# Kernel tuning notes

Measured on AMD Instinct MI355X. Metric: run time of the kernel, lower is better.

Reference implementation:

```python
import jax, jax.numpy as jnp
import numpy as np

B, S, H = 2, 2048, 1024
NH, HD = 16, 64
WIN = 256
EPS = 1e-5


def _layernorm(x, g, b):
    # normalize over last dim (head_dim)
    m = jnp.mean(x, axis=-1, keepdims=True)
    v = jnp.mean((x - m) ** 2, axis=-1, keepdims=True)
    return (x - m) * jax.lax.rsqrt(v + EPS) * g + b


def setup_inputs() -> dict:
    key = jax.random.key(0)
    ks = jax.random.split(key, 6)
    scale = 1.0 / np.sqrt(2.0 * H)  # ~ xavier_uniform with gain 1/sqrt(2)
    inp = {
        "x": jax.random.normal(ks[0], (B, S, H), dtype=jnp.float32),
        "Wq": jax.random.normal(ks[1], (H, H), dtype=jnp.float32) * scale,
        "bq": jnp.zeros((H,), jnp.float32),
        "Wk": jax.random.normal(ks[2], (H, H), dtype=jnp.float32) * scale,
        "bk": jnp.zeros((H,), jnp.float32),
        "Wv": jax.random.normal(ks[3], (H, H), dtype=jnp.float32) * scale,
        "bv": jnp.zeros((H,), jnp.float32),
        "Wo": jax.random.normal(ks[4], (H, H), dtype=jnp.float32) * scale,
        "bo": jnp.zeros((H,), jnp.float32),
        "ln_q_w": jnp.ones((HD,), jnp.float32),
        "ln_q_b": jnp.zeros((HD,), jnp.float32),
        "ln_k_w": jnp.ones((HD,), jnp.float32),
        "ln_k_b": jnp.zeros((HD,), jnp.float32),
    }
    return inp


def reference(x, Wq, bq, Wk, bk, Wv, bv, Wo, bo, ln_q_w, ln_q_b, ln_k_w, ln_k_b):
    b, s, _ = x.shape
    # projections (torch Linear: x @ W.T + b)
    q = (x @ Wq.T + bq).reshape(b, s, NH, HD)
    k = (x @ Wk.T + bk).reshape(b, s, NH, HD)
    v = (x @ Wv.T + bv).reshape(b, s, NH, HD)
    # QK layernorm over head_dim
    q = _layernorm(q, ln_q_w, ln_q_b)
    k = _layernorm(k, ln_k_w, ln_k_b)
    # scores [b, h, s, s]
    scores = jnp.einsum("bqhd,bkhd->bhqk", q, k) / np.sqrt(HD).astype(np.float32)
    i = jnp.arange(s)[:, None]
    j = jnp.arange(s)[None, :]
    mask = (j <= i) & (i - j <= WIN)
    scores = jnp.where(mask[None, None], scores, -jnp.inf)
    probs = jax.nn.softmax(scores, axis=-1)
    out = jnp.einsum("bhqk,bkhd->bqhd", probs, v).reshape(b, s, NH * HD)
    return out @ Wo.T + bo
```

## Files before the change

### kernel.cpp

```cpp
#include <hip/hip_runtime.h>
#include <hip/hip_bf16.h>
#include <cstdint>

typedef __hip_bfloat16 bf16;
typedef __attribute__((ext_vector_type(8))) short s16x8;
typedef __attribute__((ext_vector_type(4))) float f32x4;

#define NB_B 2
#define NB_S 2048
#define NB_H 1024
#define NB_NH 16
#define NB_HD 64
#define NB_WIN 256
#define NTOK 4096

static __device__ __forceinline__ unsigned pack_bf16(float a, float b) {
    bf16 ta = __float2bfloat16(a), tb = __float2bfloat16(b);
    return (unsigned)*(unsigned short*)&ta | ((unsigned)*(unsigned short*)&tb << 16);
}
static __device__ __forceinline__ unsigned short bf16u(float a) {
    bf16 t = __float2bfloat16(a);
    return *(unsigned short*)&t;
}

#define VMCNT(n) asm volatile("s_waitcnt vmcnt(" #n ")" ::: "memory")
#define SBAR __builtin_amdgcn_s_barrier()
#define LGKM0 do { asm volatile("s_waitcnt lgkmcnt(0)" ::: "memory"); \
                   __builtin_amdgcn_sched_barrier(0); } while (0)

__global__ void k_castall(const float* __restrict__ x, const float* __restrict__ Wq,
                          const float* __restrict__ Wk, const float* __restrict__ Wv,
                          const float* __restrict__ Wo,
                          bf16* __restrict__ xb, bf16* __restrict__ wqkvb,
                          bf16* __restrict__ wob) {
    int idx = blockIdx.x * blockDim.x + threadIdx.x;
    const float* in; bf16* out; int i;
    if (idx < 1048576)        { in = x;  out = xb;              i = idx * 4; }
    else if (idx < 1310720)   { in = Wq; out = wqkvb;           i = (idx - 1048576) * 4; }
    else if (idx < 1572864)   { in = Wk; out = wqkvb + 1048576; i = (idx - 1310720) * 4; }
    else if (idx < 1835008)   { in = Wv; out = wqkvb + 2097152; i = (idx - 1572864) * 4; }
    else                      { in = Wo; out = wob;             i = (idx - 1835008) * 4; }
    const float4 v = *(const float4*)(in + i);
    ushort4 u;
    u.x = bf16u(v.x); u.y = bf16u(v.y); u.z = bf16u(v.z); u.w = bf16u(v.w);
    *(ushort4*)((unsigned short*)out + i) = u;
}

#define GQ_STAGE(AD, BD, KT)                                                         \
    do {                                                                             \
        _Pragma("unroll")                                                            \
        for (int it_ = 0; it_ < 2; ++it_) {                                          \
            int c_ = it_ * 256 + tid;                                                \
            int row_ = c_ >> 2, pc_ = c_ & 3;                                        \
            int col_ = pc_ << 3;                                                     \
            __builtin_amdgcn_global_load_lds(                                        \
                (const __attribute__((address_space(1))) void*)(Ap + (size_t)(m0 + row_) * 1024 + (KT) + col_), \
                (__attribute__((address_space(3))) void*)((AD) + c_ * 8), 16, 0, 0); \
            __builtin_amdgcn_global_load_lds(                                        \
                (const __attribute__((address_space(1))) void*)(Bp + (size_t)(n0 + row_) * 1024 + (KT) + col_), \
                (__attribute__((address_space(3))) void*)((BD) + c_ * 8), 16, 0, 0); \
        }                                                                            \
        __builtin_amdgcn_sched_barrier(0);                                           \
    } while (0)

#define GQ_COMPUTE(AS, BS)                                                           \
    do {                                                                             \
        s16x8 af_[4], bf_[4];                                                        \
        _Pragma("unroll")                                                            \
        for (int mi_ = 0; mi_ < 4; ++mi_)                                            \
            af_[mi_] = *(const s16x8*)&(AS)[(wr * 64 + mi_ * 16 + q) * 32 + g * 8];  \
        _Pragma("unroll")                                                            \
        for (int ni_ = 0; ni_ < 4; ++ni_)                                            \
            bf_[ni_] = *(const s16x8*)&(BS)[(wc * 64 + ni_ * 16 + q) * 32 + g * 8];  \
        LGKM0;                                                                       \
        __builtin_amdgcn_s_setprio(1);                                               \
        _Pragma("unroll")                                                            \
        for (int mi_ = 0; mi_ < 4; ++mi_)                                            \
            _Pragma("unroll")                                                        \
            for (int ni_ = 0; ni_ < 4; ++ni_)                                        \
                acc[mi_][ni_] = __builtin_amdgcn_mfma_f32_16x16x32_bf16(             \
                    af_[mi_], bf_[ni_], acc[mi_][ni_], 0, 0, 0);                     \
        __builtin_amdgcn_s_setprio(0);                                               \
    } while (0)

#define GQ_MAINLOOP                                                                  \
    GQ_STAGE(As0, Bs0, 0);                                                           \
    GQ_STAGE(As1, Bs1, 32);                                                          \
    for (int i_ = 0; i_ < 15; ++i_) {                                                \
        const int kt_ = i_ * 64;                                                     \
        VMCNT(4); SBAR;                                                              \
        GQ_COMPUTE(As0, Bs0);                                                        \
        SBAR;                                                                        \
        GQ_STAGE(As0, Bs0, kt_ + 64);                                                \
        VMCNT(4); SBAR;                                                              \
        GQ_COMPUTE(As1, Bs1);                                                        \
        SBAR;                                                                        \
        GQ_STAGE(As1, Bs1, kt_ + 96);                                                \
    }                                                                                \
    VMCNT(4); SBAR;                                                                  \
    GQ_COMPUTE(As0, Bs0);                                                            \
    VMCNT(0); SBAR;                                                                  \
    GQ_COMPUTE(As1, Bs1)

__global__ __launch_bounds__(256, 4) void k_gemm_qkv(const bf16* __restrict__ Ap,
                                                  const bf16* __restrict__ Bp,
                                                  const float* __restrict__ bq,
                                                  const float* __restrict__ bk,
                                                  const float* __restrict__ bv,
                                                  const float* __restrict__ lqw,
                                                  const float* __restrict__ lqb,
                                                  const float* __restrict__ lkw,
                                                  const float* __restrict__ lkb,
                                                  bf16* __restrict__ qbuf,
                                                  bf16* __restrict__ kbuf,
                                                  bf16* __restrict__ vtb) {
    __shared__ bf16 As0[128 * 32], As1[128 * 32];
    __shared__ bf16 Bs0[128 * 32], Bs1[128 * 32];
    const int tid = threadIdx.x;
    const int lane = tid & 63;
    const int w = tid >> 6;
    const int wr = w >> 1, wc = w & 1;

    const int orig = blockIdx.y * gridDim.x + blockIdx.x;
    const int wk = (orig & 7) * 96 + (orig >> 3);
    const int m0 = (wk / 24) * 128, n0 = (wk % 24) * 128;

    const int g = lane >> 4, q = lane & 15;

    f32x4 acc[4][4] = {};

    GQ_MAINLOOP;

    const int col0 = n0 + wc * 64;
    const int hh = col0 >> 6;
    const int csub = col0 & 1023;
    const float* bias = (hh < 16) ? bq : (hh < 32) ? bk : bv;

    float bcol[4];
#pragma unroll
    for (int ni = 0; ni < 4; ++ni) bcol[ni] = bias[csub + ni * 16 + q];
#pragma unroll
    for (int mi = 0; mi < 4; ++mi)
#pragma unroll
        for (int ni = 0; ni < 4; ++ni)
#pragma unroll
            for (int r = 0; r < 4; ++r) acc[mi][ni][r] += bcol[ni];

    if (hh < 32) {
        const float* gwa = (hh < 16) ? lqw : lkw;
        const float* gba = (hh < 16) ? lqb : lkb;
        float gam[4], bet[4];
#pragma unroll
        for (int ni = 0; ni < 4; ++ni) {
            gam[ni] = gwa[ni * 16 + q];
            bet[ni] = gba[ni * 16 + q];
        }
        bf16* outp = (hh < 16) ? qbuf : kbuf;
#pragma unroll
        for (int mi = 0; mi < 4; ++mi)
#pragma unroll
            for (int r = 0; r < 4; ++r) {
                float s1 = acc[mi][0][r] + acc[mi][1][r] + acc[mi][2][r] + acc[mi][3][r];
                float s2 = acc[mi][0][r] * acc[mi][0][r] + acc[mi][1][r] * acc[mi][1][r]
                         + acc[mi][2][r] * acc[mi][2][r] + acc[mi][3][r] * acc[mi][3][r];
#pragma unroll
                for (int mm = 1; mm < 16; mm <<= 1) {
                    s1 += __shfl_xor(s1, mm, 64);
                    s2 += __shfl_xor(s2, mm, 64);
                }
                float mean = s1 * (1.f / 64.f);
                float var = s2 * (1.f / 64.f) - mean * mean;
                float rs = rsqrtf(var + 1e-5f);
                int token = m0 + wr * 64 + mi * 16 + g * 4 + r;
#pragma unroll
                for (int ni = 0; ni < 4; ++ni) {
                    float y = (acc[mi][ni][r] - mean) * rs * gam[ni] + bet[ni];
                    outp[(size_t)token * 1024 + csub + ni * 16 + q] = __float2bfloat16(y);
                }
            }
    } else {
        const int b = m0 >> 11;
        const int bh = b * 16 + (csub >> 6);
        const int sbase0 = (m0 & 2047) + wr * 64 + g * 4;
#pragma unroll
        for (int mi = 0; mi < 4; ++mi) {
            const int sb = sbase0 + mi * 16;
#pragma unroll
            for (int ni = 0; ni < 4; ++ni) {
                const int d = ni * 16 + q;
                ushort4 u;
                u.x = bf16u(acc[mi][ni][0]); u.y = bf16u(acc[mi][ni][1]);
                u.z = bf16u(acc[mi][ni][2]); u.w = bf16u(acc[mi][ni][3]);
                *(ushort4*)(vtb + ((size_t)bh * 64 + d) * 2048 + sb) = u;
            }
        }
    }
}

#define GO_STAGE(AD, BD, KT)                                                         \
    do {                                                                             \
        _Pragma("unroll")                                                            \
        for (int it_ = 0; it_ < 2; ++it_) {                                          \
            int c_ = it_ * 256 + tid;                                                \
            int row_ = c_ >> 2, pc_ = c_ & 3;                                        \
            int col_ = pc_ << 3;                                                     \
            __builtin_amdgcn_global_load_lds(                                        \
                (const __attribute__((address_space(1))) void*)(Ap + (size_t)(m0 + row_) * 1024 + (KT) + col_), \
                (__attribute__((address_space(3))) void*)((AD) + c_ * 8), 16, 0, 0); \
        }                                                                            \
        {                                                                            \
            int row_ = tid >> 2, pc_ = tid & 3;                                      \
            int col_ = pc_ << 3;                                                     \
            __builtin_amdgcn_global_load_lds(                                        \
                (const __attribute__((address_space(1))) void*)(Bp + (size_t)(n0 + row_) * 1024 + (KT) + col_), \
                (__attribute__((address_space(3))) void*)((BD) + tid * 8), 16, 0, 0); \
        }                                                                            \
        __builtin_amdgcn_sched_barrier(0);                                           \
    } while (0)

#define GO_COMPUTE(AS, BS)                                                           \
    do {                                                                             \
        s16x8 af_[4], bf_[2];                                                        \
        _Pragma("unroll")                                                            \
        for (int mi_ = 0; mi_ < 4; ++mi_)                                            \
            af_[mi_] = *(const s16x8*)&(AS)[(wr * 64 + mi_ * 16 + q) * 32 + g * 8];  \
        _Pragma("unroll")                                                            \
        for (int ni_ = 0; ni_ < 2; ++ni_)                                            \
            bf_[ni_] = *(const s16x8*)&(BS)[(wc * 32 + ni_ * 16 + q) * 32 + g * 8];  \
        LGKM0;                                                                       \
        __builtin_amdgcn_s_setprio(1);                                               \
        _Pragma("unroll")                                                            \
        for (int mi_ = 0; mi_ < 4; ++mi_)                                            \
            _Pragma("unroll")                                                        \
            for (int ni_ = 0; ni_ < 2; ++ni_)                                        \
                acc[mi_][ni_] = __builtin_amdgcn_mfma_f32_16x16x32_bf16(             \
                    af_[mi_], bf_[ni_], acc[mi_][ni_], 0, 0, 0);                     \
        __builtin_amdgcn_s_setprio(0);                                               \
    } while (0)

#define GO_MAINLOOP                                                                  \
    GO_STAGE(As0, Bs0, 0);                                                           \
    GO_STAGE(As1, Bs1, 32);                                                          \
    for (int i_ = 0; i_ < 15; ++i_) {                                                \
        const int kt_ = i_ * 64;                                                     \
        VMCNT(3); SBAR;                                                              \
        GO_COMPUTE(As0, Bs0);                                                        \
        SBAR;                                                                        \
        GO_STAGE(As0, Bs0, kt_ + 64);                                                \
        VMCNT(3); SBAR;                                                              \
        GO_COMPUTE(As1, Bs1);                                                        \
        SBAR;                                                                        \
        GO_STAGE(As1, Bs1, kt_ + 96);                                                \
    }                                                                                \
    VMCNT(3); SBAR;                                                                  \
    GO_COMPUTE(As0, Bs0);                                                            \
    VMCNT(0); SBAR;                                                                  \
    GO_COMPUTE(As1, Bs1)

__global__ __launch_bounds__(256, 4) void k_gemm_out(const bf16* __restrict__ Ap,
                                                  const bf16* __restrict__ Bp,
                                                  const float* __restrict__ bias,
                                                  float* __restrict__ Cv) {
    __shared__ bf16 As0[128 * 32], As1[128 * 32];
    __shared__ bf16 Bs0[64 * 32], Bs1[64 * 32];
    const int tid = threadIdx.x;
    const int lane = tid & 63;
    const int w = tid >> 6;
    const int wr = w >> 1, wc = w & 1;

    const int orig = blockIdx.y * gridDim.x + blockIdx.x;
    const int wk = (orig & 7) * 64 + (orig >> 3);
    const int m0 = (wk / 16) * 128, n0 = (wk % 16) * 64;

    const int g = lane >> 4, q = lane & 15;

    f32x4 acc[4][2] = {};

    GO_MAINLOOP;

#pragma unroll
    for (int mi = 0; mi < 4; ++mi)
#pragma unroll
        for (int ni = 0; ni < 2; ++ni) {
            int colg = n0 + wc * 32 + ni * 16 + q;
            float bcol = bias[colg];
#pragma unroll
            for (int r = 0; r < 4; ++r) {
                int rowg = m0 + wr * 64 + mi * 16 + g * 4 + r;
                Cv[(size_t)rowg * 1024 + colg] = acc[mi][ni][r] + bcol;
            }
        }
}

#undef GQ_STAGE
#undef GQ_COMPUTE
#undef GQ_MAINLOOP
#undef GO_STAGE
#undef GO_COMPUTE
#undef GO_MAINLOOP

__global__ __launch_bounds__(256) void k_attn(const bf16* __restrict__ qb,
                                              const bf16* __restrict__ kb,
                                              const bf16* __restrict__ vt,
                                              bf16* __restrict__ att) {
    __shared__ bf16 Ks[2][32 * 64];
    __shared__ bf16 Vs[2][64 * 32];

    const int orig = blockIdx.y * gridDim.x + blockIdx.x;
    const int wk = (orig & 7) * 128 + (orig >> 3);
    const int q0 = (wk & 31) * 64;
    const int bh = wk >> 5;

    const int b = bh >> 4, h = bh & 15;
    const int tid = threadIdx.x;
    const int w = tid >> 6;
    const int lane = tid & 63;
    const int g = lane >> 4, qi = lane & 15;
    const int qw0 = q0 + w * 16;
    const int iq = qw0 + qi;

    const size_t qbase = ((size_t)(b * 2048 + iq)) * 1024 + h * 64 + g * 8;
    s16x8 bq0 = *(const s16x8*)(qb + qbase);
    s16x8 bq1 = *(const s16x8*)(qb + qbase + 32);

    f32x4 o[4] = {};
    float lp = 0.f;

    int jmin = q0 - NB_WIN; if (jmin < 0) jmin = 0;
    const int c0 = jmin >> 5;
    const int c1 = (q0 + 63) >> 5;

    const int krow = tid >> 3, kpc = tid & 7;
    const int kcol = ((kpc ^ (krow & 7)) << 3);
    const int vrow = tid >> 2, vpc = tid & 3;
    const int vcol = ((vpc ^ (vrow & 3)) << 3);
    const bf16* kbase = kb + ((size_t)(b * 2048 + krow)) * 1024 + h * 64 + kcol;
    const bf16* vbase = vt + ((size_t)bh * 64 + vrow) * 2048 + vcol;

    __builtin_amdgcn_global_load_lds(
        (const __attribute__((address_space(1))) void*)(kbase + (size_t)(c0 * 32) * 1024),
        (__attribute__((address_space(3))) void*)(&Ks[0][tid * 8]), 16, 0, 0);
    __builtin_amdgcn_global_load_lds(
        (const __attribute__((address_space(1))) void*)(vbase + c0 * 32),
        (__attribute__((address_space(3))) void*)(&Vs[0][tid * 8]), 16, 0, 0);

    int buf = 0;
    for (int c = c0; c <= c1; ++c) {
        const int ks = c * 32;
        if (c < c1) {
            const int ksn = ks + 32;
            __builtin_amdgcn_global_load_lds(
                (const __attribute__((address_space(1))) void*)(kbase + (size_t)ksn * 1024),
                (__attribute__((address_space(3))) void*)(&Ks[buf ^ 1][tid * 8]), 16, 0, 0);
            __builtin_amdgcn_global_load_lds(
                (const __attribute__((address_space(1))) void*)(vbase + ksn),
                (__attribute__((address_space(3))) void*)(&Vs[buf ^ 1][tid * 8]), 16, 0, 0);
            __builtin_amdgcn_sched_barrier(0);
            VMCNT(2);
        } else {
            VMCNT(0);
        }
        SBAR;

        if (ks + 31 >= qw0 - NB_WIN && ks <= qw0 + 15) {
            const int ch0 = ((g ^ (qi & 7)) << 3);
            const bf16* kr0 = &Ks[buf][qi * 64];
            const bf16* kr1 = &Ks[buf][(16 + qi) * 64];
            s16x8 a00 = *(const s16x8*)(kr0 + ch0);
            s16x8 a01 = *(const s16x8*)(kr0 + (ch0 ^ 32));
            s16x8 a10 = *(const s16x8*)(kr1 + ch0);
            s16x8 a11 = *(const s16x8*)(kr1 + (ch0 ^ 32));

            f32x4 s0 = {}, s1 = {};
            s0 = __builtin_amdgcn_mfma_f32_16x16x32_bf16(a00, bq0, s0, 0, 0, 0);
            s0 = __builtin_amdgcn_mfma_f32_16x16x32_bf16(a01, bq1, s0, 0, 0, 0);
            s1 = __builtin_amdgcn_mfma_f32_16x16x32_bf16(a10, bq0, s1, 0, 0, 0);
            s1 = __builtin_amdgcn_mfma_f32_16x16x32_bf16(a11, bq1, s1, 0, 0, 0);

            float p0[4], p1[4];
#pragma unroll
            for (int r = 0; r < 4; ++r) {
                int j0 = ks + 4 * g + r, j1 = j0 + 16;
                p0[r] = ((unsigned)(iq - j0) <= (unsigned)NB_WIN)
                            ? __expf(s0[r] * 0.125f - 8.f) : 0.f;
                p1[r] = ((unsigned)(iq - j1) <= (unsigned)NB_WIN)
                            ? __expf(s1[r] * 0.125f - 8.f) : 0.f;
                lp += p0[r] + p1[r];
            }
            unsigned P0 = pack_bf16(p0[0], p0[1]), P1 = pack_bf16(p0[2], p0[3]);
            unsigned Q0 = pack_bf16(p1[0], p1[1]), Q1 = pack_bf16(p1[2], p1[3]);

            const int srcA = qi + (g & 1) * 32;
            const int srcB = srcA + 16;
            unsigned tP0a = __shfl((int)P0, srcA, 64), tQ0a = __shfl((int)Q0, srcA, 64);
            unsigned tP1a = __shfl((int)P1, srcA, 64), tQ1a = __shfl((int)Q1, srcA, 64);
            unsigned tP0b = __shfl((int)P0, srcB, 64), tQ0b = __shfl((int)Q0, srcB, 64);
            unsigned tP1b = __shfl((int)P1, srcB, 64), tQ1b = __shfl((int)Q1, srcB, 64);
            union { s16x8 v; unsigned u[4]; } pa;
            pa.u[0] = (g < 2) ? tP0a : tQ0a;
            pa.u[1] = (g < 2) ? tP1a : tQ1a;
            pa.u[2] = (g < 2) ? tP0b : tQ0b;
            pa.u[3] = (g < 2) ? tP1b : tQ1b;

            const int chv = ((g ^ (qi & 3)) << 3);
#pragma unroll
            for (int db = 0; db < 4; ++db) {
                s16x8 bv = *(const s16x8*)&Vs[buf][(db * 16 + qi) * 32 + chv];
                o[db] = __builtin_amdgcn_mfma_f32_16x16x32_bf16(pa.v, bv, o[db], 0, 0, 0);
            }
        }

        SBAR;
        buf ^= 1;
    }

    float l2 = lp + __shfl_xor(lp, 16, 64);
    float lf = l2 + __shfl_xor(l2, 32, 64);
    float lr[4];
#pragma unroll
    for (int r = 0; r < 4; ++r) lr[r] = __shfl(lf, 4 * g + r, 64);

#pragma unroll
    for (int db = 0; db < 4; ++db)
#pragma unroll
        for (int r = 0; r < 4; ++r) {
            float vlu = o[db][r] / lr[r];
            att[((size_t)(b * 2048 + qw0 + 4 * g + r)) * 1024 + h * 64 + db * 16 + qi] =
                __float2bfloat16(vlu);
        }
}

extern "C" void kernel_launch(void* const* d_in, const int* in_sizes, int n_in,
                              void* d_out, int out_size, void* d_ws, size_t ws_size,
                              hipStream_t stream) {
    const float* x   = (const float*)d_in[0];
    const float* Wq  = (const float*)d_in[1];
    const float* bq  = (const float*)d_in[2];
    const float* Wk  = (const float*)d_in[3];
    const float* bk  = (const float*)d_in[4];
    const float* Wv  = (const float*)d_in[5];
    const float* bv  = (const float*)d_in[6];
    const float* Wo  = (const float*)d_in[7];
    const float* bo  = (const float*)d_in[8];
    const float* lqw = (const float*)d_in[9];
    const float* lqb = (const float*)d_in[10];
    const float* lkw = (const float*)d_in[11];
    const float* lkb = (const float*)d_in[12];

    char* ws = (char*)d_ws;
    bf16* xb    = (bf16*)(ws + 0);
    bf16* wqkvb = (bf16*)(ws + 8388608);
    bf16* wob   = (bf16*)(ws + 14680064);
    bf16* qbuf  = (bf16*)(ws + 16777216);
    bf16* kbuf  = (bf16*)(ws + 25165824);
    bf16* vtb   = (bf16*)(ws + 33554432);
    bf16* attb  = (bf16*)(ws + 41943040);

    k_castall<<<8192, 256, 0, stream>>>(x, Wq, Wk, Wv, Wo, xb, wqkvb, wob);

    k_gemm_qkv<<<dim3(24, 32), 256, 0, stream>>>(xb, wqkvb, bq, bk, bv,
                                                 lqw, lqb, lkw, lkb,
                                                 qbuf, kbuf, vtb);

    k_attn<<<dim3(32, 32), 256, 0, stream>>>(qbuf, kbuf, vtb, attb);

    k_gemm_out<<<dim3(16, 32), 256, 0, stream>>>(attb, wob, bo, (float*)d_out);
}
```

Before: 90.27 us.

## Triple-buffer GEMM LDS pipeline and XOR-swizzle tiles to avoid bank conflicts

Both the QKV and output-projection GEMMs move from a double-buffered to a triple-buffered LDS ring. The next tile load is issued before computing the current one, which keeps more global loads in flight. The global-to-LDS copy and the fragment reads now use an XOR swizzle on the 16-byte chunk index to cut LDS bank conflicts. The extra LDS per block lowers the QKV kernel's occupancy bound from 4 to 3 blocks, and the ring index arithmetic adds some loop overhead.

```diff
diff --git a/kernel.cpp b/kernel.cpp
--- a/kernel.cpp
+++ b/kernel.cpp
@@ -52,7 +52,7 @@
         for (int it_ = 0; it_ < 2; ++it_) {                                          \
             int c_ = it_ * 256 + tid;                                                \
             int row_ = c_ >> 2, pc_ = c_ & 3;                                        \
-            int col_ = pc_ << 3;                                                     \
+            int col_ = (pc_ ^ ((row_ >> 1) & 3)) << 3;                               \
             __builtin_amdgcn_global_load_lds(                                        \
                 (const __attribute__((address_space(1))) void*)(Ap + (size_t)(m0 + row_) * 1024 + (KT) + col_), \
                 (__attribute__((address_space(3))) void*)((AD) + c_ * 8), 16, 0, 0); \
@@ -65,13 +65,14 @@
 
 #define GQ_COMPUTE(AS, BS)                                                           \
     do {                                                                             \
+        const int chv_ = (g ^ ((q >> 1) & 3)) << 3;                                  \
         s16x8 af_[4], bf_[4];                                                        \
         _Pragma("unroll")                                                            \
         for (int mi_ = 0; mi_ < 4; ++mi_)                                            \
-            af_[mi_] = *(const s16x8*)&(AS)[(wr * 64 + mi_ * 16 + q) * 32 + g * 8];  \
+            af_[mi_] = *(const s16x8*)&(AS)[(wr * 64 + mi_ * 16 + q) * 32 + chv_];   \
         _Pragma("unroll")                                                            \
         for (int ni_ = 0; ni_ < 4; ++ni_)                                            \
-            bf_[ni_] = *(const s16x8*)&(BS)[(wc * 64 + ni_ * 16 + q) * 32 + g * 8];  \
+            bf_[ni_] = *(const s16x8*)&(BS)[(wc * 64 + ni_ * 16 + q) * 32 + chv_];   \
         LGKM0;                                                                       \
         __builtin_amdgcn_s_setprio(1);                                               \
         _Pragma("unroll")                                                            \
@@ -83,26 +84,28 @@
         __builtin_amdgcn_s_setprio(0);                                               \
     } while (0)
 
-#define GQ_MAINLOOP                                                                  \
-    GQ_STAGE(As0, Bs0, 0);                                                           \
-    GQ_STAGE(As1, Bs1, 32);                                                          \
-    for (int i_ = 0; i_ < 15; ++i_) {                                                \
-        const int kt_ = i_ * 64;                                                     \
+#define GQ_MAINLOOP(NT)                                                              \
+    GQ_STAGE(Asb + 0 * ABUF, Bsb + 0 * BBUF, 0);                                     \
+    GQ_STAGE(Asb + 1 * ABUF, Bsb + 1 * BBUF, 32);                                    \
+    {                                                                                \
+        int bc_ = 0, bs_ = 2;                                                        \
+        for (int t_ = 0; t_ < (NT) - 2; ++t_) {                                      \
+            GQ_STAGE(Asb + bs_ * ABUF, Bsb + bs_ * BBUF, (t_ + 2) * 32);             \
+            VMCNT(8); SBAR;                                                          \
+            GQ_COMPUTE(Asb + bc_ * ABUF, Bsb + bc_ * BBUF);                          \
+            SBAR;                                                                    \
+            bc_ = (bc_ + 1 == 3) ? 0 : bc_ + 1;                                      \
+            bs_ = (bs_ + 1 == 3) ? 0 : bs_ + 1;                                      \
+        }                                                                            \
         VMCNT(4); SBAR;                                                              \
-        GQ_COMPUTE(As0, Bs0);                                                        \
+        GQ_COMPUTE(Asb + bc_ * ABUF, Bsb + bc_ * BBUF);                              \
         SBAR;                                                                        \
-        GQ_STAGE(As0, Bs0, kt_ + 64);                                                \
-        VMCNT(4); SBAR;                                                              \
-        GQ_COMPUTE(As1, Bs1);                                                        \
-        SBAR;                                                                        \
-        GQ_STAGE(As1, Bs1, kt_ + 96);                                                \
-    }                                                                                \
-    VMCNT(4); SBAR;                                                                  \
-    GQ_COMPUTE(As0, Bs0);                                                            \
-    VMCNT(0); SBAR;                                                                  \
-    GQ_COMPUTE(As1, Bs1)
-
-__global__ __launch_bounds__(256, 4) void k_gemm_qkv(const bf16* __restrict__ Ap,
+        bc_ = (bc_ + 1 == 3) ? 0 : bc_ + 1;                                          \
+        VMCNT(0); SBAR;                                                              \
+        GQ_COMPUTE(Asb + bc_ * ABUF, Bsb + bc_ * BBUF);                              \
+    }
+
+__global__ __launch_bounds__(256, 3) void k_gemm_qkv(const bf16* __restrict__ Ap,
                                                   const bf16* __restrict__ Bp,
                                                   const float* __restrict__ bq,
                                                   const float* __restrict__ bk,
@@ -114,8 +117,9 @@
                                                   bf16* __restrict__ qbuf,
                                                   bf16* __restrict__ kbuf,
                                                   bf16* __restrict__ vtb) {
-    __shared__ bf16 As0[128 * 32], As1[128 * 32];
-    __shared__ bf16 Bs0[128 * 32], Bs1[128 * 32];
+    const int ABUF = 128 * 32, BBUF = 128 * 32;
+    __shared__ bf16 Asb[3 * 128 * 32];
+    __shared__ bf16 Bsb[3 * 128 * 32];
     const int tid = threadIdx.x;
     const int lane = tid & 63;
     const int w = tid >> 6;
@@ -129,7 +133,7 @@
 
     f32x4 acc[4][4] = {};
 
-    GQ_MAINLOOP;
+    GQ_MAINLOOP(32);
 
     const int col0 = n0 + wc * 64;
     const int hh = col0 >> 6;
@@ -203,14 +207,14 @@
         for (int it_ = 0; it_ < 2; ++it_) {                                          \
             int c_ = it_ * 256 + tid;                                                \
             int row_ = c_ >> 2, pc_ = c_ & 3;                                        \
-            int col_ = pc_ << 3;                                                     \
+            int col_ = (pc_ ^ ((row_ >> 1) & 3)) << 3;                               \
             __builtin_amdgcn_global_load_lds(                                        \
                 (const __attribute__((address_space(1))) void*)(Ap + (size_t)(m0 + row_) * 1024 + (KT) + col_), \
                 (__attribute__((address_space(3))) void*)((AD) + c_ * 8), 16, 0, 0); \
         }                                                                            \
         {                                                                            \
             int row_ = tid >> 2, pc_ = tid & 3;                                      \
-            int col_ = pc_ << 3;                                                     \
+            int col_ = (pc_ ^ ((row_ >> 1) & 3)) << 3;                               \
             __builtin_amdgcn_global_load_lds(                                        \
                 (const __attribute__((address_space(1))) void*)(Bp + (size_t)(n0 + row_) * 1024 + (KT) + col_), \
                 (__attribute__((address_space(3))) void*)((BD) + tid * 8), 16, 0, 0); \
@@ -220,13 +224,14 @@
 
 #define GO_COMPUTE(AS, BS)                                                           \
     do {                                                                             \
+        const int chv_ = (g ^ ((q >> 1) & 3)) << 3;                                  \
         s16x8 af_[4], bf_[2];                                                        \
         _Pragma("unroll")                                                            \
         for (int mi_ = 0; mi_ < 4; ++mi_)                                            \
-            af_[mi_] = *(const s16x8*)&(AS)[(wr * 64 + mi_ * 16 + q) * 32 + g * 8];  \
+            af_[mi_] = *(const s16x8*)&(AS)[(wr * 64 + mi_ * 16 + q) * 32 + chv_];   \
         _Pragma("unroll")                                                            \
         for (int ni_ = 0; ni_ < 2; ++ni_)                                            \
-            bf_[ni_] = *(const s16x8*)&(BS)[(wc * 32 + ni_ * 16 + q) * 32 + g * 8];  \
+            bf_[ni_] = *(const s16x8*)&(BS)[(wc * 32 + ni_ * 16 + q) * 32 + chv_];   \
         LGKM0;                                                                       \
         __builtin_amdgcn_s_setprio(1);                                               \
         _Pragma("unroll")                                                            \
@@ -238,31 +243,34 @@
         __builtin_amdgcn_s_setprio(0);                                               \
     } while (0)
 
-#define GO_MAINLOOP                                                                  \
-    GO_STAGE(As0, Bs0, 0);                                                           \
-    GO_STAGE(As1, Bs1, 32);                                                          \
-    for (int i_ = 0; i_ < 15; ++i_) {                                                \
-        const int kt_ = i_ * 64;                                                     \
+#define GO_MAINLOOP(NT)                                                              \
+    GO_STAGE(Asb + 0 * ABUF, Bsb + 0 * BBUF, 0);                                     \
+    GO_STAGE(Asb + 1 * ABUF, Bsb + 1 * BBUF, 32);                                    \
+    {                                                                                \
+        int bc_ = 0, bs_ = 2;                                                        \
+        for (int t_ = 0; t_ < (NT) - 2; ++t_) {                                      \
+            GO_STAGE(Asb + bs_ * ABUF, Bsb + bs_ * BBUF, (t_ + 2) * 32);             \
+            VMCNT(6); SBAR;                                                          \
+            GO_COMPUTE(Asb + bc_ * ABUF, Bsb + bc_ * BBUF);                          \
+            SBAR;                                                                    \
+            bc_ = (bc_ + 1 == 3) ? 0 : bc_ + 1;                                      \
+            bs_ = (bs_ + 1 == 3) ? 0 : bs_ + 1;                                      \
+        }                                                                            \
         VMCNT(3); SBAR;                                                              \
-        GO_COMPUTE(As0, Bs0);                                                        \
+        GO_COMPUTE(Asb + bc_ * ABUF, Bsb + bc_ * BBUF);                              \
         SBAR;                                                                        \
-        GO_STAGE(As0, Bs0, kt_ + 64);                                                \
-        VMCNT(3); SBAR;                                                              \
-        GO_COMPUTE(As1, Bs1);                                                        \
-        SBAR;                                                                        \
-        GO_STAGE(As1, Bs1, kt_ + 96);                                                \
-    }                                                                                \
-    VMCNT(3); SBAR;                                                                  \
-    GO_COMPUTE(As0, Bs0);                                                            \
-    VMCNT(0); SBAR;                                                                  \
-    GO_COMPUTE(As1, Bs1)
+        bc_ = (bc_ + 1 == 3) ? 0 : bc_ + 1;                                          \
+        VMCNT(0); SBAR;                                                              \
+        GO_COMPUTE(Asb + bc_ * ABUF, Bsb + bc_ * BBUF);                              \
+    }
 
 __global__ __launch_bounds__(256, 4) void k_gemm_out(const bf16* __restrict__ Ap,
                                                   const bf16* __restrict__ Bp,
                                                   const float* __restrict__ bias,
                                                   float* __restrict__ Cv) {
-    __shared__ bf16 As0[128 * 32], As1[128 * 32];
-    __shared__ bf16 Bs0[64 * 32], Bs1[64 * 32];
+    const int ABUF = 128 * 32, BBUF = 64 * 32;
+    __shared__ bf16 Asb[3 * 128 * 32];
+    __shared__ bf16 Bsb[3 * 64 * 32];
     const int tid = threadIdx.x;
     const int lane = tid & 63;
     const int w = tid >> 6;
@@ -276,7 +284,7 @@
 
     f32x4 acc[4][2] = {};
 
-    GO_MAINLOOP;
+    GO_MAINLOOP(32);
 
 #pragma unroll
     for (int mi = 0; mi < 4; ++mi)
```

New measurement: 90.74 us. No clear change (+0.5%).
